# Kernel tuning notes

Hardware: AMD Instinct MI355X
Metric: run time of the kernel (lower is better)

Reference implementation:

```python
import jax, jax.numpy as jnp
import numpy as np
from jax import lax

B, S, H, K = 4, 4096, 2048, 4

def setup_inputs() -> dict:
    key = jax.random.key(0)
    k1, k2 = jax.random.split(key)
    hidden_states = jax.random.normal(k1, (B, S, H), dtype=jnp.float32)
    weight = jax.random.normal(k2, (H, K), dtype=jnp.float32)  # depthwise conv weight [H, k]
    attention_mask_2d = jnp.ones((B, S), dtype=jnp.float32)
    return {"hidden_states": hidden_states, "weight": weight, "attention_mask_2d": attention_mask_2d}

def reference(hidden_states, weight, attention_mask_2d):
    # Causal depthwise conv1d: left-pad k-1, groups == channels.
    h = hidden_states.shape[-1]
    k = weight.shape[-1]
    x = jnp.transpose(hidden_states, (0, 2, 1))  # [B, H, S]
    y = lax.conv_general_dilated(
        x,
        weight[:, None, :],          # [H, 1, k] (O, I/groups, W)
        window_strides=(1,),
        padding=[(k - 1, 0)],        # causal left pad
        feature_group_count=h,
        dimension_numbers=("NCH", "OIH", "NCH"),
    )
    y = jnp.transpose(y, (0, 2, 1))  # [B, S, H]
    return y * attention_mask_2d[:, :, None]
```

## Files before the change

### kernel.cpp

```cpp
#include <hip/hip_runtime.h>


constexpr int B_   = 4;
constexpr int S_   = 4096;
constexpr int H_   = 2048;
constexpr int H4_  = H_ / 4;
constexpr int TPB  = 256;
constexpr int NBLK = 2048;
constexpr int NXCD = 8;
constexpr long TOT4   = (long)B_ * S_ * H4_;
constexpr long STRIDE = (long)NBLK * TPB;

typedef float f32x4 __attribute__((ext_vector_type(4)));

__global__ __launch_bounds__(TPB, 6) void budgie_dwconv1d_kernel(
    const float* __restrict__ x,
    const float* __restrict__ w,
    const float* __restrict__ mask,
    float* __restrict__ y)
{
    const int wid = (blockIdx.x & (NXCD - 1)) * (NBLK / NXCD) + (blockIdx.x >> 3);

    const float4* __restrict__ x4 = (const float4*)x;
    const float4* __restrict__ w4 = (const float4*)w;
    f32x4* __restrict__ y4 = (f32x4*)y;

    const long g0 = (long)wid * TPB + threadIdx.x;

    const int h4    = (int)(g0 & (H4_ - 1));
    const int hbase = h4 * 4;
    const float4 w0 = w4[hbase + 0];
    const float4 w1 = w4[hbase + 1];
    const float4 w2 = w4[hbase + 2];
    const float4 w3 = w4[hbase + 3];

    const float4 zero4 = make_float4(0.f, 0.f, 0.f, 0.f);

    #pragma unroll 2
    for (long g = g0; g < TOT4; g += STRIDE) {
        const int row = (int)(g >> 9);
        const int s   = row & (S_ - 1);

        const float4 x0 = x4[g];
        float4 x1, x2, x3;
        if (s >= 3) {
            x1 = x4[g - 1 * H4_];
            x2 = x4[g - 2 * H4_];
            x3 = x4[g - 3 * H4_];
        } else {
            x1 = (s >= 1) ? x4[g - 1 * H4_] : zero4;
            x2 = (s >= 2) ? x4[g - 2 * H4_] : zero4;
            x3 = zero4;
        }

        const int  row_u = __builtin_amdgcn_readfirstlane(row);
        const float m    = mask[row_u];

        f32x4 o;
        o.x = fmaf(x3.x, w0.x, fmaf(x2.x, w0.y, fmaf(x1.x, w0.z, x0.x * w0.w)));
        o.y = fmaf(x3.y, w1.x, fmaf(x2.y, w1.y, fmaf(x1.y, w1.z, x0.y * w1.w)));
        o.z = fmaf(x3.z, w2.x, fmaf(x2.z, w2.y, fmaf(x1.z, w2.z, x0.z * w2.w)));
        o.w = fmaf(x3.w, w3.x, fmaf(x2.w, w3.y, fmaf(x1.w, w3.z, x0.w * w3.w)));
        o.x *= m; o.y *= m; o.z *= m; o.w *= m;

        __builtin_nontemporal_store(o, &y4[g]);
    }
}

extern "C" void kernel_launch(void* const* d_in, const int* in_sizes, int n_in,
                              void* d_out, int out_size, void* d_ws, size_t ws_size,
                              hipStream_t stream) {
    const float* x    = (const float*)d_in[0];
    const float* w    = (const float*)d_in[1];
    const float* mask = (const float*)d_in[2];
    float* y = (float*)d_out;

    budgie_dwconv1d_kernel<<<dim3(NBLK), TPB, 0, stream>>>(x, w, mask, y);
}
```

Baseline: 272.2 us.

## Process 8-row chunks per thread with register reuse and software prefetch

Each thread now owns one float4 column and walks 8 consecutive sequence rows, loading 11 rows (3 halo plus 8) instead of 4 loads per output, so input reads drop from 4x to about 1.4x. The next chunk is loaded into a second register buffer before the current one is consumed, separated by a scheduling barrier to overlap memory latency with compute and stores. Block size becomes 512 threads with 512 blocks and a fixed iteration count. Register pressure rises from the two 11-element float4 buffers, which may lower occupancy.

```diff
diff --git a/kernel.cpp b/kernel.cpp
--- a/kernel.cpp
+++ b/kernel.cpp
@@ -4,57 +4,47 @@
 constexpr int B_   = 4;
 constexpr int S_   = 4096;
 constexpr int H_   = 2048;
-constexpr int H4_  = H_ / 4;
-constexpr int TPB  = 256;
-constexpr int NBLK = 2048;
+constexpr int H4   = H_ / 4;
+constexpr int TPB  = 512;
+constexpr int ROWS = 8;
+constexpr int NCH  = B_ * S_ / ROWS;
+constexpr int NBLK = 512;
+constexpr int ITER = NCH / NBLK;
 constexpr int NXCD = 8;
-constexpr long TOT4   = (long)B_ * S_ * H4_;
-constexpr long STRIDE = (long)NBLK * TPB;
 
 typedef float f32x4 __attribute__((ext_vector_type(4)));
 
-__global__ __launch_bounds__(TPB, 6) void budgie_dwconv1d_kernel(
-    const float* __restrict__ x,
-    const float* __restrict__ w,
-    const float* __restrict__ mask,
-    float* __restrict__ y)
-{
-    const int wid = (blockIdx.x & (NXCD - 1)) * (NBLK / NXCD) + (blockIdx.x >> 3);
+struct Buf { float4 v[ROWS + 3]; };
 
-    const float4* __restrict__ x4 = (const float4*)x;
-    const float4* __restrict__ w4 = (const float4*)w;
-    f32x4* __restrict__ y4 = (f32x4*)y;
+__device__ __forceinline__ void load_chunk(Buf& d, int r0, int s0, int t,
+                                           const float4* __restrict__ x4) {
+    const long a = (long)r0 * H4 + t;
+    if (s0 != 0) {
+        #pragma unroll
+        for (int j = 0; j < 3; ++j) d.v[j] = x4[a + (long)(j - 3) * H4];
+    } else {
+        const float4 z = make_float4(0.f, 0.f, 0.f, 0.f);
+        #pragma unroll
+        for (int j = 0; j < 3; ++j) d.v[j] = z;
+    }
+    #pragma unroll
+    for (int j = 0; j < ROWS; ++j) d.v[3 + j] = x4[a + (long)j * H4];
+}
 
-    const long g0 = (long)wid * TPB + threadIdx.x;
-
-    const int h4    = (int)(g0 & (H4_ - 1));
-    const int hbase = h4 * 4;
-    const float4 w0 = w4[hbase + 0];
-    const float4 w1 = w4[hbase + 1];
-    const float4 w2 = w4[hbase + 2];
-    const float4 w3 = w4[hbase + 3];
-
-    const float4 zero4 = make_float4(0.f, 0.f, 0.f, 0.f);
-
-    #pragma unroll 2
-    for (long g = g0; g < TOT4; g += STRIDE) {
-        const int row = (int)(g >> 9);
-        const int s   = row & (S_ - 1);
-
-        const float4 x0 = x4[g];
-        float4 x1, x2, x3;
-        if (s >= 3) {
-            x1 = x4[g - 1 * H4_];
-            x2 = x4[g - 2 * H4_];
-            x3 = x4[g - 3 * H4_];
-        } else {
-            x1 = (s >= 1) ? x4[g - 1 * H4_] : zero4;
-            x2 = (s >= 2) ? x4[g - 2 * H4_] : zero4;
-            x3 = zero4;
-        }
-
-        const int  row_u = __builtin_amdgcn_readfirstlane(row);
-        const float m    = mask[row_u];
+__device__ __forceinline__ void consume_chunk(const Buf& c, int r0, int t,
+                                              const float4& w0, const float4& w1,
+                                              const float4& w2, const float4& w3,
+                                              const float* __restrict__ mask,
+                                              f32x4* __restrict__ y4) {
+    const long a   = (long)r0 * H4 + t;
+    const int  r0u = __builtin_amdgcn_readfirstlane(r0);
+    #pragma unroll
+    for (int tr = 0; tr < ROWS; ++tr) {
+        const float4 x3 = c.v[tr + 0];
+        const float4 x2 = c.v[tr + 1];
+        const float4 x1 = c.v[tr + 2];
+        const float4 x0 = c.v[tr + 3];
+        const float  m  = mask[r0u + tr];
 
         f32x4 o;
         o.x = fmaf(x3.x, w0.x, fmaf(x2.x, w0.y, fmaf(x1.x, w0.z, x0.x * w0.w)));
@@ -63,7 +53,52 @@
         o.w = fmaf(x3.w, w3.x, fmaf(x2.w, w3.y, fmaf(x1.w, w3.z, x0.w * w3.w)));
         o.x *= m; o.y *= m; o.z *= m; o.w *= m;
 
-        __builtin_nontemporal_store(o, &y4[g]);
+        __builtin_nontemporal_store(o, y4 + a + (long)tr * H4);
+    }
+}
+
+__global__ __launch_bounds__(TPB, 4) void budgie_dwconv1d_kernel(
+    const float* __restrict__ x,
+    const float* __restrict__ w,
+    const float* __restrict__ mask,
+    float* __restrict__ y)
+{
+    const int t = threadIdx.x;
+
+    const int bswz = (blockIdx.x & (NXCD - 1)) * (NBLK / NXCD) + (blockIdx.x >> 3);
+
+    const float4* __restrict__ x4 = (const float4*)x;
+    const float4* __restrict__ w4 = (const float4*)w;
+    f32x4* __restrict__ y4 = (f32x4*)y;
+
+    const float4 w0 = w4[t * 4 + 0];
+    const float4 w1 = w4[t * 4 + 1];
+    const float4 w2 = w4[t * 4 + 2];
+    const float4 w3 = w4[t * 4 + 3];
+
+    Buf A, Bv;
+
+    {
+        const int r0 = bswz * ROWS;
+        load_chunk(A, r0, r0 & (S_ - 1), t, x4);
+    }
+
+    #pragma unroll
+    for (int i = 0; i < ITER; ++i) {
+        const int r0 = (i * NBLK + bswz) * ROWS;
+
+        if (i + 1 < ITER) {
+            const int r0n = ((i + 1) * NBLK + bswz) * ROWS;
+            load_chunk(Bv, r0n, r0n & (S_ - 1), t, x4);
+        }
+        __builtin_amdgcn_sched_barrier(0);
+
+        consume_chunk(A, r0, t, w0, w1, w2, w3, mask, y4);
+
+        if (i + 1 < ITER) {
+            #pragma unroll
+            for (int j = 0; j < ROWS + 3; ++j) A.v[j] = Bv.v[j];
+        }
     }
 }
 
```

After: 236.2 us. 1.15x faster.

## Stage row tiles through LDS with double buffering and reuse causal history

Applied to the files above, without the earlier changes.

Each block now owns a span of 32 consecutive sequence rows. It streams 4-row tiles of the input into shared memory with global_load_lds, double-buffered so the next tile loads while the current one is computed. The three previous rows needed by the causal filter are carried in registers between tiles, so each input element is read from global memory about once instead of up to four times. The price is 64KB of LDS per block, lower occupancy and hand-written vmcnt waits whose correctness depends on how loads and stores are ordered.

```diff
diff --git a/kernel.cpp b/kernel.cpp
--- a/kernel.cpp
+++ b/kernel.cpp
@@ -1,69 +1,119 @@
 #include <hip/hip_runtime.h>
+#include <stdint.h>
 
 
-constexpr int B_   = 4;
-constexpr int S_   = 4096;
-constexpr int H_   = 2048;
-constexpr int H4_  = H_ / 4;
-constexpr int TPB  = 256;
-constexpr int NBLK = 2048;
-constexpr int NXCD = 8;
-constexpr long TOT4   = (long)B_ * S_ * H4_;
-constexpr long STRIDE = (long)NBLK * TPB;
+constexpr int B_    = 4;
+constexpr int S_    = 4096;
+constexpr int H_    = 2048;
+constexpr int H4    = H_ / 4;
+constexpr int TPB   = 512;
+constexpr int TROWS = 4;
+constexpr int TILE4 = TROWS * H4;
+constexpr int SPANR = 32;
+constexpr int NT    = SPANR / TROWS;
+constexpr int NBLK  = B_ * S_ / SPANR;
 
 typedef float f32x4 __attribute__((ext_vector_type(4)));
 
-__global__ __launch_bounds__(TPB, 6) void budgie_dwconv1d_kernel(
+__device__ __forceinline__ void stage_tile(const float4* gsrc, float4* lbuf,
+                                           int wv, int ln) {
+    #pragma unroll
+    for (int j = 0; j < 4; ++j) {
+        const int fo = (wv * 4 + j) * 64;
+        __builtin_amdgcn_global_load_lds(
+            (const __attribute__((address_space(1))) void*)(gsrc + fo + ln),
+            (__attribute__((address_space(3))) void*)(lbuf + fo),
+            16, 0, 0);
+    }
+}
+
+__device__ __forceinline__ f32x4 conv_row(const float4& x3, const float4& x2,
+                                          const float4& x1, const float4& x0,
+                                          const float4& w0, const float4& w1,
+                                          const float4& w2, const float4& w3,
+                                          float m) {
+    f32x4 o;
+    o.x = fmaf(x3.x, w0.x, fmaf(x2.x, w0.y, fmaf(x1.x, w0.z, x0.x * w0.w)));
+    o.y = fmaf(x3.y, w1.x, fmaf(x2.y, w1.y, fmaf(x1.y, w1.z, x0.y * w1.w)));
+    o.z = fmaf(x3.z, w2.x, fmaf(x2.z, w2.y, fmaf(x1.z, w2.z, x0.z * w2.w)));
+    o.w = fmaf(x3.w, w3.x, fmaf(x2.w, w3.y, fmaf(x1.w, w3.z, x0.w * w3.w)));
+    o.x *= m; o.y *= m; o.z *= m; o.w *= m;
+    return o;
+}
+
+__global__ __launch_bounds__(TPB, 4) void budgie_dwconv1d_kernel(
     const float* __restrict__ x,
     const float* __restrict__ w,
     const float* __restrict__ mask,
     float* __restrict__ y)
 {
-    const int wid = (blockIdx.x & (NXCD - 1)) * (NBLK / NXCD) + (blockIdx.x >> 3);
+    __shared__ float4 buf[2][TILE4];
 
-    const float4* __restrict__ x4 = (const float4*)x;
-    const float4* __restrict__ w4 = (const float4*)w;
-    f32x4* __restrict__ y4 = (f32x4*)y;
+    const int t  = threadIdx.x;
+    const int wv = t >> 6;
+    const int ln = t & 63;
+    const int r0 = blockIdx.x * SPANR;
 
-    const long g0 = (long)wid * TPB + threadIdx.x;
+    const float4* x4 = (const float4*)x;
+    const float4* w4 = (const float4*)w;
+    f32x4* y4 = (f32x4*)y;
 
-    const int h4    = (int)(g0 & (H4_ - 1));
-    const int hbase = h4 * 4;
-    const float4 w0 = w4[hbase + 0];
-    const float4 w1 = w4[hbase + 1];
-    const float4 w2 = w4[hbase + 2];
-    const float4 w3 = w4[hbase + 3];
+    const float4 w0 = w4[t * 4 + 0];
+    const float4 w1 = w4[t * 4 + 1];
+    const float4 w2 = w4[t * 4 + 2];
+    const float4 w3 = w4[t * 4 + 3];
 
     const float4 zero4 = make_float4(0.f, 0.f, 0.f, 0.f);
 
-    #pragma unroll 2
-    for (long g = g0; g < TOT4; g += STRIDE) {
-        const int row = (int)(g >> 9);
-        const int s   = row & (S_ - 1);
+    float4 h1, h2, h3;
+    if (r0 >= 3) {
+        h1 = x4[(long)(r0 - 1) * H4 + t];
+        h2 = x4[(long)(r0 - 2) * H4 + t];
+        h3 = x4[(long)(r0 - 3) * H4 + t];
+    } else {
+        h1 = h2 = h3 = zero4;
+    }
 
-        const float4 x0 = x4[g];
-        float4 x1, x2, x3;
-        if (s >= 3) {
-            x1 = x4[g - 1 * H4_];
-            x2 = x4[g - 2 * H4_];
-            x3 = x4[g - 3 * H4_];
+    stage_tile(x4 + (long)r0 * H4, buf[0], wv, ln);
+    asm volatile("s_waitcnt vmcnt(0)" ::: "memory");
+    __builtin_amdgcn_sched_barrier(0);
+    __builtin_amdgcn_s_barrier();
+
+    for (int i = 0; i < NT; ++i) {
+        const int R = r0 + i * TROWS;
+        const int p = i & 1;
+
+        if (i + 1 < NT) {
+            stage_tile(x4 + (long)(R + TROWS) * H4, buf[1 - p], wv, ln);
+            asm volatile("s_waitcnt vmcnt(8)" ::: "memory");
         } else {
-            x1 = (s >= 1) ? x4[g - 1 * H4_] : zero4;
-            x2 = (s >= 2) ? x4[g - 2 * H4_] : zero4;
-            x3 = zero4;
+            asm volatile("s_waitcnt vmcnt(4)" ::: "memory");
         }
+        __builtin_amdgcn_sched_barrier(0);
+        __builtin_amdgcn_s_barrier();
 
-        const int  row_u = __builtin_amdgcn_readfirstlane(row);
-        const float m    = mask[row_u];
+        const float4 L0 = buf[p][0 * H4 + t];
+        const float4 L1 = buf[p][1 * H4 + t];
+        const float4 L2 = buf[p][2 * H4 + t];
+        const float4 L3 = buf[p][3 * H4 + t];
 
-        f32x4 o;
-        o.x = fmaf(x3.x, w0.x, fmaf(x2.x, w0.y, fmaf(x1.x, w0.z, x0.x * w0.w)));
-        o.y = fmaf(x3.y, w1.x, fmaf(x2.y, w1.y, fmaf(x1.y, w1.z, x0.y * w1.w)));
-        o.z = fmaf(x3.z, w2.x, fmaf(x2.z, w2.y, fmaf(x1.z, w2.z, x0.z * w2.w)));
-        o.w = fmaf(x3.w, w3.x, fmaf(x2.w, w3.y, fmaf(x1.w, w3.z, x0.w * w3.w)));
-        o.x *= m; o.y *= m; o.z *= m; o.w *= m;
+        if ((R & (S_ - 1)) == 0) { h1 = h2 = h3 = zero4; }
 
-        __builtin_nontemporal_store(o, &y4[g]);
+        const int Ru = __builtin_amdgcn_readfirstlane(R);
+
+        f32x4 o0 = conv_row(h3, h2, h1, L0, w0, w1, w2, w3, mask[Ru + 0]);
+        f32x4 o1 = conv_row(h2, h1, L0, L1, w0, w1, w2, w3, mask[Ru + 1]);
+        f32x4 o2 = conv_row(h1, L0, L1, L2, w0, w1, w2, w3, mask[Ru + 2]);
+        f32x4 o3 = conv_row(L0, L1, L2, L3, w0, w1, w2, w3, mask[Ru + 3]);
+
+        __builtin_nontemporal_store(o0, y4 + (long)(R + 0) * H4 + t);
+        __builtin_nontemporal_store(o1, y4 + (long)(R + 1) * H4 + t);
+        __builtin_nontemporal_store(o2, y4 + (long)(R + 2) * H4 + t);
+        __builtin_nontemporal_store(o3, y4 + (long)(R + 3) * H4 + t);
+
+        h1 = L3; h2 = L2; h3 = L1;
+
+        __builtin_amdgcn_s_barrier();
     }
 }
 
```

Measured after the change: 239.1 us. 1.14x faster.
